# Kernel tuning notes

Measured on AMD Instinct MI355X. Metric: run time of the kernel, lower is better.

The kernel has to match this reference:

```python
import jax, jax.numpy as jnp
import numpy as np

N, C, T, V, K = 64, 64, 300, 25, 3
EPS = 1e-5


def setup_inputs() -> dict:
    key = jax.random.key(0)
    ks = jax.random.split(key, 4)
    x = jax.random.normal(ks[0], (N, C, T, V), dtype=jnp.float32)
    A = jax.random.uniform(ks[1], (K, V, V), dtype=jnp.float32)
    # per-subset 1x1 conv weights: W[k] maps C_in -> C_out, plus bias b[k]
    W = jax.random.normal(ks[2], (K, C, C), dtype=jnp.float32) * (1.0 / np.sqrt(C))
    b = jax.random.normal(ks[3], (K, C), dtype=jnp.float32) * 0.01
    gamma = jnp.ones((C,), dtype=jnp.float32)
    beta = jnp.zeros((C,), dtype=jnp.float32)
    return {"x": x, "A": A, "W": W, "b": b, "gamma": gamma, "beta": beta}


def reference(x, A, W, b, gamma, beta):
    # y = sum_k conv1x1_k( einsum('nctv,vw->nctw', x, A[k]) )
    # conv1x1 over (C,T,V) with kernel 1 == channel matmul; fuse subsets via one einsum.
    y = jnp.einsum('nctv,kvw,koc->notw', x, A, W)
    y = y + jnp.sum(b, axis=0)[None, :, None, None]
    # BatchNorm2d in training mode: batch statistics over (N, T, V) per channel
    mean = jnp.mean(y, axis=(0, 2, 3), keepdims=True)
    var = jnp.mean(jnp.square(y - mean), axis=(0, 2, 3), keepdims=True)
    y = gamma[None, :, None, None] * (y - mean) * jax.lax.rsqrt(var + EPS) + beta[None, :, None, None]
    # residual (in_channels == out_channels -> identity) + relu
    return jax.nn.relu(y + x)
```

## Files before the change

kernel.cpp:

```cpp
#include <hip/hip_runtime.h>
#include <hip/hip_bf16.h>

#define N_ 64
#define C_ 64
#define T_ 300
#define V_ 25
#define K_ 3
#define TT 12
#define NTILE 25
#define NBLK 1600
#define XROW 384
#define WP 72
#define AP 33
#define EPS_ 1e-5f

typedef __bf16 bf16_t;
typedef __bf16 bf16x4 __attribute__((ext_vector_type(4)));
typedef __bf16 bf16x8 __attribute__((ext_vector_type(8)));
typedef float f32x4 __attribute__((ext_vector_type(4)));

static __device__ __forceinline__ bf16_t tobf(float f) { return (bf16_t)f; }
static __device__ __forceinline__ int emask(int c) { return ((c & 3) << 3) | ((c & 8) << 2); }

union SmemU {
  struct { bf16_t W[3 * 64 * WP]; bf16_t A[3 * 32 * AP + 8]; } wa;
  bf16_t xs[64 * XROW];
};

struct Frags {
  bf16x8 wfrag[6];
  bf16x8 afrag[3][2];
  int fK[4], fS5[4];
  float bs[4];
  int obase;
};

static __device__ __forceinline__ void stage_wa(
    const float* __restrict__ A, const float* __restrict__ W, SmemU& sm, int tid) {
  for (int m = tid; m < 3072; m += 256) {
    f32x4 v4 = *(reinterpret_cast<const f32x4*>(W) + m);
    int f = m << 2;
    int k = f >> 12, o = (f >> 6) & 63, c = f & 63;
    bf16x4 h;
    h[0] = tobf(v4[0]); h[1] = tobf(v4[1]); h[2] = tobf(v4[2]); h[3] = tobf(v4[3]);
    *reinterpret_cast<bf16x4*>(&sm.wa.W[(k * 64 + o) * WP + c]) = h;
  }
  for (int f = tid; f < 1875; f += 256) {
    int k = f / 625, r = f - k * 625;
    int v = r / 25, w = r - v * 25;
    sm.wa.A[(k * 32 + v) * AP + w] = tobf(A[f]);
  }
}

static __device__ __forceinline__ void read_frags(
    const SmemU& sm, const float* __restrict__ b, int wv, int l15, int lg, Frags& F) {
  const int o = wv * 16 + l15;
  #pragma unroll
  for (int k = 0; k < 3; ++k)
    #pragma unroll
    for (int ch = 0; ch < 2; ++ch)
      F.wfrag[k * 2 + ch] =
          *reinterpret_cast<const bf16x8*>(&sm.wa.W[(k * 64 + o) * WP + ch * 32 + lg * 8]);
  #pragma unroll
  for (int k = 0; k < 3; ++k)
    #pragma unroll
    for (int wh = 0; wh < 2; ++wh) {
      int w = wh * 16 + l15;
      bf16x8 f;
      #pragma unroll
      for (int j = 0; j < 8; ++j) {
        int v = lg * 8 + j;
        bf16_t val = sm.wa.A[(k * 32 + v) * AP + w];
        f[j] = (v < V_ && w < V_) ? val : tobf(0.f);
      }
      F.afrag[k][wh] = f;
    }
  const int crow = 8 * (l15 >> 2) + (l15 & 3);
  #pragma unroll
  for (int q = 0; q < 4; ++q) {
    int c = ((q >> 1) * 32) + ((q & 1) * 4) + crow;
    int em = emask(c);
    F.fK[q] = c * XROW + ((lg * 8) ^ (em & 24));
    F.fS5[q] = em & 32;
  }
  F.obase = wv * 16 + lg * 4;
  #pragma unroll
  for (int r = 0; r < 4; ++r)
    F.bs[r] = b[F.obase + r] + b[64 + F.obase + r] + b[128 + F.obase + r];
}

static __device__ __forceinline__ void stage_x(
    const float* __restrict__ x, SmemU& sm, int n, int t0, int tid) {
  for (int i = tid; i < 64 * TT * 7; i += 256) {
    int c = i / (TT * 7);
    int r = i - c * (TT * 7);
    int t = r / 7, v = 25 + (r - t * 7);
    sm.xs[c * XROW + (((t << 5) + v) ^ emask(c))] = tobf(0.f);
  }
  const float* xb = x + (size_t)n * 480000 + (size_t)t0 * 25;
  for (int m = tid; m < 4800; m += 256) {
    int c = m / 75, q = m - c * 75;
    f32x4 fv = *reinterpret_cast<const f32x4*>(xb + (size_t)c * 7500 + 4 * q);
    int e = 4 * q;
    int t = e / 25, v = e - t * 25;
    int em = emask(c);
    #pragma unroll
    for (int i2 = 0; i2 < 4; ++i2) {
      sm.xs[c * XROW + (((t << 5) + v) ^ em)] = tobf(fv[i2]);
      if (++v == 25) { v = 0; ++t; }
    }
  }
}

static __device__ __forceinline__ void compute_t(
    const bf16_t* xs, const Frags& F, int t, int wh, f32x4& acc0, f32x4& acc1) {
  bf16x8 xf[4];
  #pragma unroll
  for (int q = 0; q < 4; ++q)
    xf[q] = *reinterpret_cast<const bf16x8*>(xs + F.fK[q] + ((t << 5) ^ F.fS5[q]));
  acc0 = f32x4{0.f, 0.f, 0.f, 0.f};
  acc1 = f32x4{0.f, 0.f, 0.f, 0.f};
  #pragma unroll
  for (int k = 0; k < 3; ++k) {
    #pragma unroll
    for (int ch = 0; ch < 2; ++ch) {
      f32x4 zero = {0.f, 0.f, 0.f, 0.f};
      f32x4 dP = __builtin_amdgcn_mfma_f32_16x16x32_bf16(xf[ch * 2 + 0], F.afrag[k][wh], zero, 0, 0, 0);
      f32x4 dQ = __builtin_amdgcn_mfma_f32_16x16x32_bf16(xf[ch * 2 + 1], F.afrag[k][wh], zero, 0, 0, 0);
      bf16x8 zf;
      zf[0] = tobf(dP[0]); zf[1] = tobf(dP[1]); zf[2] = tobf(dP[2]); zf[3] = tobf(dP[3]);
      zf[4] = tobf(dQ[0]); zf[5] = tobf(dQ[1]); zf[6] = tobf(dQ[2]); zf[7] = tobf(dQ[3]);
      if (ch == 0)
        acc0 = __builtin_amdgcn_mfma_f32_16x16x32_bf16(F.wfrag[k * 2 + ch], zf, acc0, 0, 0, 0);
      else
        acc1 = __builtin_amdgcn_mfma_f32_16x16x32_bf16(F.wfrag[k * 2 + ch], zf, acc1, 0, 0, 0);
    }
  }
}

__global__ __launch_bounds__(256, 3) void k1_stats(
    const float* __restrict__ x, const float* __restrict__ A,
    const float* __restrict__ W, const float* __restrict__ b,
    float* __restrict__ part) {
  __shared__ __align__(16) SmemU sm;
  __shared__ float stats[2][64];

  const int bid = (blockIdx.x & 7) * (NBLK / 8) + (blockIdx.x >> 3);
  const int n = bid / NTILE;
  const int t0 = (bid - n * NTILE) * TT;
  const int tid = threadIdx.x;
  const int lane = tid & 63;
  const int wv = tid >> 6;
  const int l15 = lane & 15;
  const int lg = lane >> 4;

  stage_wa(A, W, sm, tid);
  __syncthreads();
  Frags F;
  read_frags(sm, b, wv, l15, lg, F);
  __syncthreads();
  stage_x(x, sm, n, t0, tid);
  __syncthreads();

  float lsum[4] = {0.f, 0.f, 0.f, 0.f}, lsq[4] = {0.f, 0.f, 0.f, 0.f};
  const int w_lo = l15, w_hi = 16 + l15;

  #pragma unroll 2
  for (int t = 0; t < TT; ++t) {
    #pragma unroll
    for (int wh = 0; wh < 2; ++wh) {
      f32x4 acc0, acc1;
      compute_t(sm.xs, F, t, wh, acc0, acc1);
      const int w = wh ? w_hi : w_lo;
      if (w < V_) {
        #pragma unroll
        for (int r = 0; r < 4; ++r) {
          float val = acc0[r] + acc1[r] + F.bs[r];
          lsum[r] += val;
          lsq[r] += val * val;
        }
      }
    }
  }

  #pragma unroll
  for (int d = 1; d < 16; d <<= 1) {
    #pragma unroll
    for (int r = 0; r < 4; ++r) {
      lsum[r] += __shfl_xor(lsum[r], d);
      lsq[r]  += __shfl_xor(lsq[r], d);
    }
  }
  if (l15 == 0) {
    #pragma unroll
    for (int r = 0; r < 4; ++r) {
      stats[0][F.obase + r] = lsum[r];
      stats[1][F.obase + r] = lsq[r];
    }
  }
  __syncthreads();
  if (tid < 128) part[(size_t)bid * 128 + tid] = stats[tid >> 6][tid & 63];
}

__global__ __launch_bounds__(256) void k2_stats(
    const float* __restrict__ part,
    const float* __restrict__ gamma, const float* __restrict__ beta,
    float* __restrict__ ss) {
  const int o = blockIdx.x;
  const int tid = threadIdx.x;
  double s = 0.0, q = 0.0;
  for (int i = tid; i < NBLK; i += 256) {
    s += (double)part[(size_t)i * 128 + o];
    q += (double)part[(size_t)i * 128 + 64 + o];
  }
  __shared__ double sd[256], qd[256];
  sd[tid] = s; qd[tid] = q;
  __syncthreads();
  for (int step = 128; step > 0; step >>= 1) {
    if (tid < step) { sd[tid] += sd[tid + step]; qd[tid] += qd[tid + step]; }
    __syncthreads();
  }
  if (tid == 0) {
    const double cnt = 480000.0;
    double mean = sd[0] / cnt;
    double var = qd[0] / cnt - mean * mean;
    float inv = rsqrtf((float)var + EPS_);
    float sc = gamma[o] * inv;
    float sh = beta[o] - (float)mean * sc;
    ss[2 * o] = sc;
    ss[2 * o + 1] = sh;
  }
}

__global__ __launch_bounds__(256, 3) void k3_apply(
    const float* __restrict__ x, const float* __restrict__ A,
    const float* __restrict__ W, const float* __restrict__ b,
    const float* __restrict__ ss, float* __restrict__ out) {
  __shared__ __align__(16) SmemU sm;

  const int bid = (blockIdx.x & 7) * (NBLK / 8) + (blockIdx.x >> 3);
  const int n = bid / NTILE;
  const int t0 = (bid - n * NTILE) * TT;
  const int tid = threadIdx.x;
  const int lane = tid & 63;
  const int wv = tid >> 6;
  const int l15 = lane & 15;
  const int lg = lane >> 4;

  stage_wa(A, W, sm, tid);
  __syncthreads();
  Frags F;
  read_frags(sm, b, wv, l15, lg, F);
  __syncthreads();
  stage_x(x, sm, n, t0, tid);

  float sc[4], sh[4];
  #pragma unroll
  for (int r = 0; r < 4; ++r) {
    sc[r] = ss[2 * (F.obase + r)];
    sh[r] = ss[2 * (F.obase + r) + 1];
  }
  __syncthreads();

  float* ob = out + (size_t)n * 480000 + (size_t)t0 * 25;
  const int w_lo = l15, w_hi = 16 + l15;

  #pragma unroll 2
  for (int t = 0; t < TT; ++t) {
    #pragma unroll
    for (int wh = 0; wh < 2; ++wh) {
      f32x4 acc0, acc1;
      compute_t(sm.xs, F, t, wh, acc0, acc1);
      const int w = wh ? w_hi : w_lo;
      if (w < V_) {
        #pragma unroll
        for (int r = 0; r < 4; ++r) {
          const int o = F.obase + r;
          float val = acc0[r] + acc1[r] + F.bs[r];
          float xr = (float)sm.xs[o * XROW + (((t << 5) + w) ^ emask(o))];
          ob[(size_t)o * 7500 + t * 25 + w] = fmaxf(sc[r] * val + sh[r] + xr, 0.f);
        }
      }
    }
  }
}

extern "C" void kernel_launch(void* const* d_in, const int* in_sizes, int n_in,
                              void* d_out, int out_size, void* d_ws, size_t ws_size,
                              hipStream_t stream) {
  const float* x     = (const float*)d_in[0];
  const float* A     = (const float*)d_in[1];
  const float* W     = (const float*)d_in[2];
  const float* b     = (const float*)d_in[3];
  const float* gamma = (const float*)d_in[4];
  const float* beta  = (const float*)d_in[5];
  float* out = (float*)d_out;

  float* part = (float*)d_ws;
  float* ss   = part + (size_t)NBLK * 128;

  k1_stats<<<NBLK, 256, 0, stream>>>(x, A, W, b, part);
  k2_stats<<<64, 256, 0, stream>>>(part, gamma, beta, ss);
  k3_apply<<<NBLK, 256, 0, stream>>>(x, A, W, b, ss, out);
}
```

Measured before the change: 147.8 us.

## Store pre-BN output in first pass and apply BN/residual in elementwise kernel

The first kernel now writes the un-normalized conv output into the output buffer while it accumulates statistics. The final kernel no longer recomputes the graph conv and MFMA chain. It becomes a simple vectorized elementwise pass that reads y and x, applies scale/shift plus the residual and ReLU, and writes in place. This trades the repeated matmul compute for an extra global write and read of the full fp32 tensor (about 123MB each way). It also vectorizes x staging into LDS with bf16x4 stores and pre-transposes A so the fragments load as single vectors.

```diff
diff --git a/kernel.cpp b/kernel.cpp
--- a/kernel.cpp
+++ b/kernel.cpp
@@ -11,19 +11,20 @@
 #define NBLK 1600
 #define XROW 384
 #define WP 72
-#define AP 33
+#define ATP 40
 #define EPS_ 1e-5f
 
 typedef __bf16 bf16_t;
 typedef __bf16 bf16x4 __attribute__((ext_vector_type(4)));
 typedef __bf16 bf16x8 __attribute__((ext_vector_type(8)));
 typedef float f32x4 __attribute__((ext_vector_type(4)));
+typedef float f32x4u __attribute__((ext_vector_type(4), aligned(4)));
 
 static __device__ __forceinline__ bf16_t tobf(float f) { return (bf16_t)f; }
 static __device__ __forceinline__ int emask(int c) { return ((c & 3) << 3) | ((c & 8) << 2); }
 
 union SmemU {
-  struct { bf16_t W[3 * 64 * WP]; bf16_t A[3 * 32 * AP + 8]; } wa;
+  struct { bf16_t W[3 * 64 * WP]; bf16_t At[3 * 32 * ATP]; } wa;
   bf16_t xs[64 * XROW];
 };
 
@@ -45,10 +46,10 @@
     h[0] = tobf(v4[0]); h[1] = tobf(v4[1]); h[2] = tobf(v4[2]); h[3] = tobf(v4[3]);
     *reinterpret_cast<bf16x4*>(&sm.wa.W[(k * 64 + o) * WP + c]) = h;
   }
-  for (int f = tid; f < 1875; f += 256) {
-    int k = f / 625, r = f - k * 625;
-    int v = r / 25, w = r - v * 25;
-    sm.wa.A[(k * 32 + v) * AP + w] = tobf(A[f]);
+  for (int i = tid; i < 3072; i += 256) {
+    int k = i >> 10, r = i & 1023, w = r >> 5, v = r & 31;
+    float val = (v < V_ && w < V_) ? A[k * 625 + v * 25 + w] : 0.f;
+    sm.wa.At[(k * 32 + w) * ATP + v] = tobf(val);
   }
 }
 
@@ -64,17 +65,9 @@
   #pragma unroll
   for (int k = 0; k < 3; ++k)
     #pragma unroll
-    for (int wh = 0; wh < 2; ++wh) {
-      int w = wh * 16 + l15;
-      bf16x8 f;
-      #pragma unroll
-      for (int j = 0; j < 8; ++j) {
-        int v = lg * 8 + j;
-        bf16_t val = sm.wa.A[(k * 32 + v) * AP + w];
-        f[j] = (v < V_ && w < V_) ? val : tobf(0.f);
-      }
-      F.afrag[k][wh] = f;
-    }
+    for (int wh = 0; wh < 2; ++wh)
+      F.afrag[k][wh] =
+          *reinterpret_cast<const bf16x8*>(&sm.wa.At[(k * 32 + wh * 16 + l15) * ATP + lg * 8]);
   const int crow = 8 * (l15 >> 2) + (l15 & 3);
   #pragma unroll
   for (int q = 0; q < 4; ++q) {
@@ -91,24 +84,21 @@
 
 static __device__ __forceinline__ void stage_x(
     const float* __restrict__ x, SmemU& sm, int n, int t0, int tid) {
-  for (int i = tid; i < 64 * TT * 7; i += 256) {
-    int c = i / (TT * 7);
-    int r = i - c * (TT * 7);
-    int t = r / 7, v = 25 + (r - t * 7);
-    sm.xs[c * XROW + (((t << 5) + v) ^ emask(c))] = tobf(0.f);
-  }
   const float* xb = x + (size_t)n * 480000 + (size_t)t0 * 25;
-  for (int m = tid; m < 4800; m += 256) {
-    int c = m / 75, q = m - c * 75;
-    f32x4 fv = *reinterpret_cast<const f32x4*>(xb + (size_t)c * 7500 + 4 * q);
-    int e = 4 * q;
-    int t = e / 25, v = e - t * 25;
-    int em = emask(c);
-    #pragma unroll
-    for (int i2 = 0; i2 < 4; ++i2) {
-      sm.xs[c * XROW + (((t << 5) + v) ^ em)] = tobf(fv[i2]);
-      if (++v == 25) { v = 0; ++t; }
-    }
+  for (int i = tid; i < 64 * TT * 8; i += 256) {
+    int c = i / (TT * 8), r = i - c * (TT * 8);
+    int t = r >> 3, vb = r & 7;
+    bf16x4 h;
+    if (vb < 6) {
+      f32x4u v4 = *reinterpret_cast<const f32x4u*>(xb + (size_t)c * 7500 + t * 25 + vb * 4);
+      h[0] = tobf(v4[0]); h[1] = tobf(v4[1]); h[2] = tobf(v4[2]); h[3] = tobf(v4[3]);
+    } else if (vb == 6) {
+      float s = xb[(size_t)c * 7500 + t * 25 + 24];
+      h[0] = tobf(s); h[1] = tobf(0.f); h[2] = tobf(0.f); h[3] = tobf(0.f);
+    } else {
+      h[0] = tobf(0.f); h[1] = tobf(0.f); h[2] = tobf(0.f); h[3] = tobf(0.f);
+    }
+    *reinterpret_cast<bf16x4*>(&sm.xs[c * XROW + (((t << 5) + vb * 4) ^ emask(c))]) = h;
   }
 }
 
@@ -138,10 +128,10 @@
   }
 }
 
-__global__ __launch_bounds__(256, 3) void k1_stats(
+__global__ __launch_bounds__(256, 3) void k1_compute(
     const float* __restrict__ x, const float* __restrict__ A,
     const float* __restrict__ W, const float* __restrict__ b,
-    float* __restrict__ part) {
+    float* __restrict__ y, float* __restrict__ part) {
   __shared__ __align__(16) SmemU sm;
   __shared__ float stats[2][64];
 
@@ -164,6 +154,7 @@
 
   float lsum[4] = {0.f, 0.f, 0.f, 0.f}, lsq[4] = {0.f, 0.f, 0.f, 0.f};
   const int w_lo = l15, w_hi = 16 + l15;
+  float* yb = y + (size_t)n * 480000 + (size_t)t0 * 25;
 
   #pragma unroll 2
   for (int t = 0; t < TT; ++t) {
@@ -178,6 +169,7 @@
           float val = acc0[r] + acc1[r] + F.bs[r];
           lsum[r] += val;
           lsq[r] += val * val;
+          yb[(size_t)(F.obase + r) * 7500 + t * 25 + w] = val;
         }
       }
     }
@@ -232,56 +224,24 @@
   }
 }
 
-__global__ __launch_bounds__(256, 3) void k3_apply(
-    const float* __restrict__ x, const float* __restrict__ A,
-    const float* __restrict__ W, const float* __restrict__ b,
-    const float* __restrict__ ss, float* __restrict__ out) {
-  __shared__ __align__(16) SmemU sm;
-
-  const int bid = (blockIdx.x & 7) * (NBLK / 8) + (blockIdx.x >> 3);
-  const int n = bid / NTILE;
-  const int t0 = (bid - n * NTILE) * TT;
-  const int tid = threadIdx.x;
-  const int lane = tid & 63;
-  const int wv = tid >> 6;
-  const int l15 = lane & 15;
-  const int lg = lane >> 4;
-
-  stage_wa(A, W, sm, tid);
-  __syncthreads();
-  Frags F;
-  read_frags(sm, b, wv, l15, lg, F);
-  __syncthreads();
-  stage_x(x, sm, n, t0, tid);
-
-  float sc[4], sh[4];
-  #pragma unroll
-  for (int r = 0; r < 4; ++r) {
-    sc[r] = ss[2 * (F.obase + r)];
-    sh[r] = ss[2 * (F.obase + r) + 1];
-  }
-  __syncthreads();
-
-  float* ob = out + (size_t)n * 480000 + (size_t)t0 * 25;
-  const int w_lo = l15, w_hi = 16 + l15;
-
-  #pragma unroll 2
-  for (int t = 0; t < TT; ++t) {
-    #pragma unroll
-    for (int wh = 0; wh < 2; ++wh) {
-      f32x4 acc0, acc1;
-      compute_t(sm.xs, F, t, wh, acc0, acc1);
-      const int w = wh ? w_hi : w_lo;
-      if (w < V_) {
-        #pragma unroll
-        for (int r = 0; r < 4; ++r) {
-          const int o = F.obase + r;
-          float val = acc0[r] + acc1[r] + F.bs[r];
-          float xr = (float)sm.xs[o * XROW + (((t << 5) + w) ^ emask(o))];
-          ob[(size_t)o * 7500 + t * 25 + w] = fmaxf(sc[r] * val + sh[r] + xr, 0.f);
-        }
-      }
-    }
+__global__ __launch_bounds__(256) void k3_finish(
+    const float* __restrict__ x, const float* __restrict__ ss,
+    float* __restrict__ y) {
+  const int p = blockIdx.x;
+  const int c = p & 63;
+  const float sc = ss[2 * c];
+  const float sh = ss[2 * c + 1];
+  const float4* xv = reinterpret_cast<const float4*>(x + (size_t)p * 7500);
+  float4* yv = reinterpret_cast<float4*>(y + (size_t)p * 7500);
+  for (int i = threadIdx.x; i < 1875; i += 256) {
+    float4 a = yv[i];
+    float4 b4 = xv[i];
+    float4 o;
+    o.x = fmaxf(sc * a.x + sh + b4.x, 0.f);
+    o.y = fmaxf(sc * a.y + sh + b4.y, 0.f);
+    o.z = fmaxf(sc * a.z + sh + b4.z, 0.f);
+    o.w = fmaxf(sc * a.w + sh + b4.w, 0.f);
+    yv[i] = o;
   }
 }
 
@@ -294,12 +254,12 @@
   const float* b     = (const float*)d_in[3];
   const float* gamma = (const float*)d_in[4];
   const float* beta  = (const float*)d_in[5];
-  float* out = (float*)d_out;
+  float* y = (float*)d_out;
 
   float* part = (float*)d_ws;
   float* ss   = part + (size_t)NBLK * 128;
 
-  k1_stats<<<NBLK, 256, 0, stream>>>(x, A, W, b, part);
+  k1_compute<<<NBLK, 256, 0, stream>>>(x, A, W, b, y, part);
   k2_stats<<<64, 256, 0, stream>>>(part, gamma, beta, ss);
-  k3_apply<<<NBLK, 256, 0, stream>>>(x, A, W, b, ss, out);
-}
+  k3_finish<<<4096, 256, 0, stream>>>(x, ss, y);
+}
```

Result: slower. 157.7 us (+6.7%).
